# Performance work log

Hardware: AMD Instinct MI355X
Metric: run time of the kernel (lower is better)

## Reference

```python
import jax, jax.numpy as jnp
import numpy as np

FP8_MAX = 448.0  # float8_e4m3fn max
EPS = 1e-6


def _rms_norm(x, w):
    # x: [T, H], w: [H]
    var = jnp.mean(x * x, axis=-1, keepdims=True)
    return x * jax.lax.rsqrt(var + EPS) * w


def _fused_add_rms_norm(x, resid, w):
    r = x + resid
    return _rms_norm(r, w), r


def _fp8_linear(y, W):
    # dynamic per-token activation quant + per-tensor weight quant, fp8 e4m3
    s = jnp.maximum(jnp.max(jnp.abs(y), axis=-1, keepdims=True) / FP8_MAX, 1e-12)  # [T,1]
    qx = jnp.clip(y / s, -FP8_MAX, FP8_MAX).astype(jnp.float8_e4m3fn).astype(jnp.float32)
    ws = jnp.maximum(jnp.max(jnp.abs(W)) / FP8_MAX, 1e-12)  # scalar
    qw = jnp.clip(W / ws, -FP8_MAX, FP8_MAX).astype(jnp.float8_e4m3fn).astype(jnp.float32)
    # out = dequant(qx) @ dequant(qw).T = (qx @ qw.T) * s * ws ; W is [out, in]
    return (qx @ qw.T) * (s * ws)


def setup_inputs() -> dict:
    key = jax.random.key(0)
    ks = jax.random.split(key, 8)
    H, T = 4096, 4096
    x = jax.random.normal(ks[0], (T, H), dtype=jnp.float32)
    nw0 = 1.0 + 0.02 * jax.random.normal(ks[1], (H,), dtype=jnp.float32)
    nw1 = 1.0 + 0.02 * jax.random.normal(ks[2], (H,), dtype=jnp.float32)
    nw2 = 1.0 + 0.02 * jax.random.normal(ks[3], (H,), dtype=jnp.float32)
    nw3 = 1.0 + 0.02 * jax.random.normal(ks[4], (H,), dtype=jnp.float32)
    W0 = 0.02 * jax.random.normal(ks[5], (H, H), dtype=jnp.float32)
    W1 = 0.02 * jax.random.normal(ks[6], (H, H), dtype=jnp.float32)
    W2 = 0.02 * jax.random.normal(ks[7], (H, H), dtype=jnp.float32)
    return {"x": x, "nw0": nw0, "nw1": nw1, "nw2": nw2, "nw3": nw3,
            "W0": W0, "W1": W1, "W2": W2}


def reference(x, nw0, nw1, nw2, nw3, W0, W1, W2):
    x = jax.nn.relu(x)
    resid = x
    y = _rms_norm(x, nw0)
    x2 = _fp8_linear(y, W0)
    y2, resid = _fused_add_rms_norm(x2, resid, nw1)
    x3 = _fp8_linear(y2, W1)
    y3, resid = _fused_add_rms_norm(x3, resid, nw2)
    x4 = _fp8_linear(y3, W2)
    y4, resid = _fused_add_rms_norm(x4, resid, nw3)
    return y4
```

## Files before the change

### kernel.cpp

```cpp
#include <hip/hip_runtime.h>
#include <cstdint>
#include <cstddef>

#define AS1 __attribute__((address_space(1)))
#define AS3 __attribute__((address_space(3)))

typedef __attribute__((ext_vector_type(4))) float f32x4;
typedef __attribute__((ext_vector_type(16))) float f32x16;
typedef __attribute__((ext_vector_type(4))) int i32x4;
typedef __attribute__((ext_vector_type(8))) int i32x8;

constexpr int HD = 4096;
constexpr float FP8MAX = 448.0f;

__device__ inline float wave_red(float v, bool ismax) {
#pragma unroll
    for (int i = 32; i > 0; i >>= 1) {
        float o = __shfl_xor(v, i, 64);
        v = ismax ? fmaxf(v, o) : (v + o);
    }
    return v;
}

__device__ inline float blk_red(float v, float* red, bool ismax) {
    v = wave_red(v, ismax);
    const int wid = threadIdx.x >> 6;
    __syncthreads();
    if ((threadIdx.x & 63) == 0) red[wid] = v;
    __syncthreads();
    float a = red[0], b = red[1], c = red[2], d = red[3];
    return ismax ? fmaxf(fmaxf(a, b), fmaxf(c, d)) : ((a + b) + (c + d));
}

__device__ inline uint32_t pack4_fp8(float a, float b, float c, float d) {
    int v = 0;
    v = __builtin_amdgcn_cvt_pk_fp8_f32(a, b, v, false);
    v = __builtin_amdgcn_cvt_pk_fp8_f32(c, d, v, true);
    return (uint32_t)v;
}

__device__ inline float clipdiv(float y, float s) {
    float t = y / s;
    t = fminf(t, FP8MAX);
    t = fmaxf(t, -FP8MAX);
    return t;
}

__global__ __launch_bounds__(256) void w_absmax(const float* __restrict__ W0,
                                                const float* __restrict__ W1,
                                                const float* __restrict__ W2,
                                                uint32_t* __restrict__ wmax) {
    __shared__ float red[4];
    const float* W = (blockIdx.z == 0) ? W0 : (blockIdx.z == 1 ? W1 : W2);
    const float4* W4 = (const float4*)W;
    const int n4 = HD * HD / 4;
    float m = 0.f;
    for (int i = blockIdx.x * blockDim.x + threadIdx.x; i < n4; i += gridDim.x * blockDim.x) {
        float4 v = W4[i];
        m = fmaxf(m, fmaxf(fmaxf(fabsf(v.x), fabsf(v.y)), fmaxf(fabsf(v.z), fabsf(v.w))));
    }
    m = blk_red(m, red, true);
    if (threadIdx.x == 0)
        atomicMax((unsigned int*)(wmax + blockIdx.z), __float_as_uint(m));
}

__global__ __launch_bounds__(256) void w_quant(const float* __restrict__ W,
                                               const uint32_t* __restrict__ wmaxbits,
                                               uint32_t* __restrict__ qw) {
    const float sw = fmaxf(__uint_as_float(*wmaxbits) / FP8MAX, 1e-12f);
    const int i = blockIdx.x * blockDim.x + threadIdx.x;
    float4 v = ((const float4*)W)[i];
    qw[i] = pack4_fp8(clipdiv(v.x, sw), clipdiv(v.y, sw), clipdiv(v.z, sw), clipdiv(v.w, sw));
}

__global__ __launch_bounds__(256) void fused_rms(const float* __restrict__ xin,
                                                 const float* __restrict__ addin,
                                                 float* __restrict__ resid_out,
                                                 const float* __restrict__ nw,
                                                 uint32_t* __restrict__ qx,
                                                 float* __restrict__ srow,
                                                 float* __restrict__ yout,
                                                 const int mode) {
    __shared__ float red[4];
    const int row = blockIdx.x;
    const int tid = threadIdx.x;
    const size_t base = (size_t)row * HD;
    const float4* xr = (const float4*)(xin + base);

    float4 v[4];
    float ss = 0.f;
    if (mode == 0) {
#pragma unroll
        for (int j = 0; j < 4; j++) {
            float4 t = xr[tid + j * 256];
            t.x = fmaxf(t.x, 0.f); t.y = fmaxf(t.y, 0.f);
            t.z = fmaxf(t.z, 0.f); t.w = fmaxf(t.w, 0.f);
            v[j] = t;
            ss += t.x * t.x + t.y * t.y + t.z * t.z + t.w * t.w;
        }
    } else {
        const float4* ar = (const float4*)(addin + base);
#pragma unroll
        for (int j = 0; j < 4; j++) {
            float4 t = xr[tid + j * 256];
            float4 a = ar[tid + j * 256];
            t.x += a.x; t.y += a.y; t.z += a.z; t.w += a.w;
            v[j] = t;
            ss += t.x * t.x + t.y * t.y + t.z * t.z + t.w * t.w;
        }
    }
    if (resid_out) {
        float4* ro = (float4*)(resid_out + base);
#pragma unroll
        for (int j = 0; j < 4; j++) ro[tid + j * 256] = v[j];
    }
    ss = blk_red(ss, red, false);
    const float rs = 1.0f / sqrtf(ss / (float)HD + 1e-6f);

    const float4* nw4 = (const float4*)nw;
    float4 y[4];
    float amax = 0.f;
#pragma unroll
    for (int j = 0; j < 4; j++) {
        float4 w = nw4[tid + j * 256];
        float4 t;
        t.x = (v[j].x * rs) * w.x; t.y = (v[j].y * rs) * w.y;
        t.z = (v[j].z * rs) * w.z; t.w = (v[j].w * rs) * w.w;
        y[j] = t;
        amax = fmaxf(amax, fmaxf(fmaxf(fabsf(t.x), fabsf(t.y)), fmaxf(fabsf(t.z), fabsf(t.w))));
    }

    if (mode == 2) {
        float4* yo = (float4*)(yout + base);
#pragma unroll
        for (int j = 0; j < 4; j++) yo[tid + j * 256] = y[j];
        return;
    }

    amax = blk_red(amax, red, true);
    const float s = fmaxf(amax / FP8MAX, 1e-12f);
    if (tid == 0) srow[row] = s;
    uint32_t* qr = qx + base / 4;
#pragma unroll
    for (int j = 0; j < 4; j++) {
        qr[tid + j * 256] = pack4_fp8(clipdiv(y[j].x, s), clipdiv(y[j].y, s),
                                      clipdiv(y[j].z, s), clipdiv(y[j].w, s));
    }
}

__global__ __launch_bounds__(256) void gemm_fp8mx(const uint8_t* __restrict__ qx,
                                                  const uint8_t* __restrict__ qw,
                                                  const float* __restrict__ srow,
                                                  const uint32_t* __restrict__ wmaxbits,
                                                  float* __restrict__ out) {
    __shared__ uint8_t As[128 * 128];
    __shared__ uint8_t Bs[128 * 128];

    const int tid = threadIdx.x;
    const int wave = tid >> 6;
    const int lane = tid & 63;
    const int lr = lane & 31;
    const int lh = lane >> 5;

    const int m0 = blockIdx.y * 128;
    const int n0 = blockIdx.x * 128;
    const int wm = (wave >> 1) * 64;
    const int wn = (wave & 1) * 64;

    f32x16 acc[2][2];
#pragma unroll
    for (int i = 0; i < 2; i++)
#pragma unroll
        for (int j = 0; j < 2; j++)
#pragma unroll
            for (int e = 0; e < 16; e++) acc[i][j][e] = 0.f;

    const int strow = wave * 8 + (lane >> 3);
    const int sg = (lane & 7) ^ (lane >> 3);
    const uint8_t* aga = qx + (size_t)(m0 + strow) * HD + sg * 16;
    const uint8_t* bga = qw + (size_t)(n0 + strow) * HD + sg * 16;
    const int ldst = wave * 1024 + lane * 16;

    for (int k0 = 0; k0 < HD; k0 += 128) {
#pragma unroll
        for (int c = 0; c < 4; c++) {
            __builtin_amdgcn_global_load_lds((const AS1 void*)(aga + (size_t)c * 32 * HD + k0),
                                             (AS3 void*)(As + c * 4096 + ldst), 16, 0, 0);
            __builtin_amdgcn_global_load_lds((const AS1 void*)(bga + (size_t)c * 32 * HD + k0),
                                             (AS3 void*)(Bs + c * 4096 + ldst), 16, 0, 0);
        }
        __syncthreads();

#pragma unroll
        for (int kh = 0; kh < 2; kh++) {
            union { i32x8 v8; i32x4 v4[2]; } af[2], bf[2];
            const int kg0 = kh * 4 + lh * 2;
#pragma unroll
            for (int i = 0; i < 2; i++) {
                const int ar = wm + i * 32 + lr;
                const uint8_t* pa = As + ar * 128;
                af[i].v4[0] = *(const i32x4*)(pa + ((kg0 ^ (ar & 7)) << 4));
                af[i].v4[1] = *(const i32x4*)(pa + (((kg0 + 1) ^ (ar & 7)) << 4));
                const int br = wn + i * 32 + lr;
                const uint8_t* pb = Bs + br * 128;
                bf[i].v4[0] = *(const i32x4*)(pb + ((kg0 ^ (br & 7)) << 4));
                bf[i].v4[1] = *(const i32x4*)(pb + (((kg0 + 1) ^ (br & 7)) << 4));
            }
#pragma unroll
            for (int i = 0; i < 2; i++)
#pragma unroll
                for (int j = 0; j < 2; j++)
                    acc[i][j] = __builtin_amdgcn_mfma_scale_f32_32x32x64_f8f6f4(
                        af[i].v8, bf[j].v8, acc[i][j],
                        0, 0,
                        0, 0x7F7F7F7Fu,
                        0, 0x7F7F7F7Fu);
        }
        __syncthreads();
    }

    const float wsc = fmaxf(__uint_as_float(*wmaxbits) / FP8MAX, 1e-12f);
#pragma unroll
    for (int i = 0; i < 2; i++) {
#pragma unroll
        for (int reg = 0; reg < 16; reg++) {
            const int row = (reg & 3) + 8 * (reg >> 2) + 4 * lh;
            const int m = m0 + wm + i * 32 + row;
            const float sv = srow[m] * wsc;
            float* orow = out + (size_t)m * HD + n0 + wn + lr;
#pragma unroll
            for (int j = 0; j < 2; j++)
                orow[j * 32] = acc[i][j][reg] * sv;
        }
    }
}

extern "C" void kernel_launch(void* const* d_in, const int* in_sizes, int n_in,
                              void* d_out, int out_size, void* d_ws, size_t ws_size,
                              hipStream_t stream) {
    const float* x   = (const float*)d_in[0];
    const float* nw0 = (const float*)d_in[1];
    const float* nw1 = (const float*)d_in[2];
    const float* nw2 = (const float*)d_in[3];
    const float* nw3 = (const float*)d_in[4];
    const float* W0  = (const float*)d_in[5];
    const float* W1  = (const float*)d_in[6];
    const float* W2  = (const float*)d_in[7];
    float* out = (float*)d_out;

    char* ws = (char*)d_ws;
    float*    resid = (float*)(ws);
    uint32_t* qx    = (uint32_t*)(ws + (size_t)67108864);
    uint32_t* qw    = (uint32_t*)(ws + (size_t)83886080);
    float*    srow  = (float*)(ws + (size_t)100663296);
    uint32_t* wmax  = (uint32_t*)(ws + (size_t)100679680);
    float*    x2    = out;

    hipMemsetAsync(wmax, 0, 12, stream);
    hipLaunchKernelGGL(w_absmax, dim3(1024, 1, 3), dim3(256), 0, stream, W0, W1, W2, wmax);

    hipLaunchKernelGGL(fused_rms, dim3(4096), dim3(256), 0, stream,
                       x, (const float*)nullptr, resid, nw0, qx, srow, (float*)nullptr, 0);

    const float* Ws[3]  = {W0, W1, W2};
    const float* nws[3] = {nw1, nw2, nw3};
    for (int l = 0; l < 3; l++) {
        hipLaunchKernelGGL(w_quant, dim3(HD * HD / 4 / 256), dim3(256), 0, stream,
                           Ws[l], wmax + l, qw);
        hipLaunchKernelGGL(gemm_fp8mx, dim3(32, 32), dim3(256), 0, stream,
                           (const uint8_t*)qx, (const uint8_t*)qw, srow, wmax + l, x2);
        if (l < 2) {
            hipLaunchKernelGGL(fused_rms, dim3(4096), dim3(256), 0, stream,
                               x2, (const float*)resid, resid, nws[l], qx, srow,
                               (float*)nullptr, 1);
        } else {
            hipLaunchKernelGGL(fused_rms, dim3(4096), dim3(256), 0, stream,
                               x2, (const float*)resid, (float*)nullptr, nws[l],
                               (uint32_t*)nullptr, (float*)nullptr, out, 2);
        }
    }
}
```

Before: 657.3 us.

## Fold weight quantization into neighbouring kernels and merge RMS reductions

Weight fp8 quantization no longer runs as a separate launch. It is appended as extra blocks to the first RMS kernel (for W0) and to each GEMM grid (for the next layer's weight), with two ping-pong weight buffers, so it overlaps with useful work. The RMS kernel also computes the activation absmax in the same reduction pass as the sum of squares, using max|x*w|*rs. This removes one block-wide sync, and quantization multiplies by a reciprocal instead of dividing. The trade-offs are that division becomes reciprocal-multiply, which can change fp8 rounding at the edges, and the overlap path needs a larger workspace. When that workspace is not available it falls back to the old schedule.

```diff
diff --git a/kernel.cpp b/kernel.cpp
--- a/kernel.cpp
+++ b/kernel.cpp
@@ -12,25 +12,6 @@
 
 constexpr int HD = 4096;
 constexpr float FP8MAX = 448.0f;
-
-__device__ inline float wave_red(float v, bool ismax) {
-#pragma unroll
-    for (int i = 32; i > 0; i >>= 1) {
-        float o = __shfl_xor(v, i, 64);
-        v = ismax ? fmaxf(v, o) : (v + o);
-    }
-    return v;
-}
-
-__device__ inline float blk_red(float v, float* red, bool ismax) {
-    v = wave_red(v, ismax);
-    const int wid = threadIdx.x >> 6;
-    __syncthreads();
-    if ((threadIdx.x & 63) == 0) red[wid] = v;
-    __syncthreads();
-    float a = red[0], b = red[1], c = red[2], d = red[3];
-    return ismax ? fmaxf(fmaxf(a, b), fmaxf(c, d)) : ((a + b) + (c + d));
-}
 
 __device__ inline uint32_t pack4_fp8(float a, float b, float c, float d) {
     int v = 0;
@@ -39,11 +20,16 @@
     return (uint32_t)v;
 }
 
-__device__ inline float clipdiv(float y, float s) {
-    float t = y / s;
+__device__ inline float clipmul(float y, float rcs) {
+    float t = y * rcs;
     t = fminf(t, FP8MAX);
     t = fmaxf(t, -FP8MAX);
     return t;
+}
+
+__device__ inline uint32_t quant4(float4 v, float rcs) {
+    return pack4_fp8(clipmul(v.x, rcs), clipmul(v.y, rcs),
+                     clipmul(v.z, rcs), clipmul(v.w, rcs));
 }
 
 __global__ __launch_bounds__(256) void w_absmax(const float* __restrict__ W0,
@@ -59,18 +45,22 @@
         float4 v = W4[i];
         m = fmaxf(m, fmaxf(fmaxf(fabsf(v.x), fabsf(v.y)), fmaxf(fabsf(v.z), fabsf(v.w))));
     }
-    m = blk_red(m, red, true);
-    if (threadIdx.x == 0)
+#pragma unroll
+    for (int i = 32; i > 0; i >>= 1) m = fmaxf(m, __shfl_xor(m, i, 64));
+    if ((threadIdx.x & 63) == 0) red[threadIdx.x >> 6] = m;
+    __syncthreads();
+    if (threadIdx.x == 0) {
+        m = fmaxf(fmaxf(red[0], red[1]), fmaxf(red[2], red[3]));
         atomicMax((unsigned int*)(wmax + blockIdx.z), __float_as_uint(m));
+    }
 }
 
 __global__ __launch_bounds__(256) void w_quant(const float* __restrict__ W,
                                                const uint32_t* __restrict__ wmaxbits,
                                                uint32_t* __restrict__ qw) {
-    const float sw = fmaxf(__uint_as_float(*wmaxbits) / FP8MAX, 1e-12f);
+    const float rsw = 1.0f / fmaxf(__uint_as_float(*wmaxbits) / FP8MAX, 1e-12f);
     const int i = blockIdx.x * blockDim.x + threadIdx.x;
-    float4 v = ((const float4*)W)[i];
-    qw[i] = pack4_fp8(clipdiv(v.x, sw), clipdiv(v.y, sw), clipdiv(v.z, sw), clipdiv(v.w, sw));
+    qw[i] = quant4(((const float4*)W)[i], rsw);
 }
 
 __global__ __launch_bounds__(256) void fused_rms(const float* __restrict__ xin,
@@ -80,23 +70,41 @@
                                                  uint32_t* __restrict__ qx,
                                                  float* __restrict__ srow,
                                                  float* __restrict__ yout,
-                                                 const int mode) {
-    __shared__ float red[4];
+                                                 const int mode,
+                                                 const float* __restrict__ Wq,
+                                                 const uint32_t* __restrict__ wqmaxbits,
+                                                 uint32_t* __restrict__ qwout) {
+    const int tid = threadIdx.x;
+    if (blockIdx.x >= 4096) {
+        const float rsw = 1.0f / fmaxf(__uint_as_float(*wqmaxbits) / FP8MAX, 1e-12f);
+        const float4* W4 = (const float4*)Wq;
+        int i = (blockIdx.x - 4096) * 256 + tid;
+#pragma unroll
+        for (int it = 0; it < 4; it++, i += 4096 * 256)
+            qwout[i] = quant4(W4[i], rsw);
+        return;
+    }
+
+    __shared__ float reds[4];
+    __shared__ float redm[4];
     const int row = blockIdx.x;
-    const int tid = threadIdx.x;
     const size_t base = (size_t)row * HD;
     const float4* xr = (const float4*)(xin + base);
-
-    float4 v[4];
-    float ss = 0.f;
+    const float4* nw4 = (const float4*)nw;
+
+    float4 v[4], w[4];
+    float ss = 0.f, pm = 0.f;
     if (mode == 0) {
 #pragma unroll
         for (int j = 0; j < 4; j++) {
             float4 t = xr[tid + j * 256];
+            w[j] = nw4[tid + j * 256];
             t.x = fmaxf(t.x, 0.f); t.y = fmaxf(t.y, 0.f);
             t.z = fmaxf(t.z, 0.f); t.w = fmaxf(t.w, 0.f);
             v[j] = t;
             ss += t.x * t.x + t.y * t.y + t.z * t.z + t.w * t.w;
+            pm = fmaxf(pm, fmaxf(fmaxf(fabsf(t.x * w[j].x), fabsf(t.y * w[j].y)),
+                                 fmaxf(fabsf(t.z * w[j].z), fabsf(t.w * w[j].w))));
         }
     } else {
         const float4* ar = (const float4*)(addin + base);
@@ -104,9 +112,12 @@
         for (int j = 0; j < 4; j++) {
             float4 t = xr[tid + j * 256];
             float4 a = ar[tid + j * 256];
+            w[j] = nw4[tid + j * 256];
             t.x += a.x; t.y += a.y; t.z += a.z; t.w += a.w;
             v[j] = t;
             ss += t.x * t.x + t.y * t.y + t.z * t.z + t.w * t.w;
+            pm = fmaxf(pm, fmaxf(fmaxf(fabsf(t.x * w[j].x), fabsf(t.y * w[j].y)),
+                                 fmaxf(fabsf(t.z * w[j].z), fabsf(t.w * w[j].w))));
         }
     }
     if (resid_out) {
@@ -114,37 +125,42 @@
 #pragma unroll
         for (int j = 0; j < 4; j++) ro[tid + j * 256] = v[j];
     }
-    ss = blk_red(ss, red, false);
+
+#pragma unroll
+    for (int i = 32; i > 0; i >>= 1) {
+        ss += __shfl_xor(ss, i, 64);
+        pm = fmaxf(pm, __shfl_xor(pm, i, 64));
+    }
+    if ((tid & 63) == 0) { reds[tid >> 6] = ss; redm[tid >> 6] = pm; }
+    __syncthreads();
+    ss = (reds[0] + reds[1]) + (reds[2] + reds[3]);
+    pm = fmaxf(fmaxf(redm[0], redm[1]), fmaxf(redm[2], redm[3]));
+
     const float rs = 1.0f / sqrtf(ss / (float)HD + 1e-6f);
-
-    const float4* nw4 = (const float4*)nw;
-    float4 y[4];
-    float amax = 0.f;
-#pragma unroll
-    for (int j = 0; j < 4; j++) {
-        float4 w = nw4[tid + j * 256];
-        float4 t;
-        t.x = (v[j].x * rs) * w.x; t.y = (v[j].y * rs) * w.y;
-        t.z = (v[j].z * rs) * w.z; t.w = (v[j].w * rs) * w.w;
-        y[j] = t;
-        amax = fmaxf(amax, fmaxf(fmaxf(fabsf(t.x), fabsf(t.y)), fmaxf(fabsf(t.z), fabsf(t.w))));
-    }
 
     if (mode == 2) {
         float4* yo = (float4*)(yout + base);
 #pragma unroll
-        for (int j = 0; j < 4; j++) yo[tid + j * 256] = y[j];
+        for (int j = 0; j < 4; j++) {
+            float4 t;
+            t.x = (v[j].x * rs) * w[j].x; t.y = (v[j].y * rs) * w[j].y;
+            t.z = (v[j].z * rs) * w[j].z; t.w = (v[j].w * rs) * w[j].w;
+            yo[tid + j * 256] = t;
+        }
         return;
     }
 
-    amax = blk_red(amax, red, true);
+    const float amax = pm * rs;
     const float s = fmaxf(amax / FP8MAX, 1e-12f);
+    const float rcs = 1.0f / s;
     if (tid == 0) srow[row] = s;
     uint32_t* qr = qx + base / 4;
 #pragma unroll
     for (int j = 0; j < 4; j++) {
-        qr[tid + j * 256] = pack4_fp8(clipdiv(y[j].x, s), clipdiv(y[j].y, s),
-                                      clipdiv(y[j].z, s), clipdiv(y[j].w, s));
+        float4 t;
+        t.x = (v[j].x * rs) * w[j].x; t.y = (v[j].y * rs) * w[j].y;
+        t.z = (v[j].z * rs) * w[j].z; t.w = (v[j].w * rs) * w[j].w;
+        qr[tid + j * 256] = quant4(t, rcs);
     }
 }
 
@@ -152,11 +168,25 @@
                                                   const uint8_t* __restrict__ qw,
                                                   const float* __restrict__ srow,
                                                   const uint32_t* __restrict__ wmaxbits,
-                                                  float* __restrict__ out) {
+                                                  float* __restrict__ out,
+                                                  const float* __restrict__ Wnext,
+                                                  const uint32_t* __restrict__ wnmaxbits,
+                                                  uint32_t* __restrict__ qwnext) {
     __shared__ uint8_t As[128 * 128];
     __shared__ uint8_t Bs[128 * 128];
 
     const int tid = threadIdx.x;
+
+    if (blockIdx.z == 1) {
+        const float rsw = 1.0f / fmaxf(__uint_as_float(*wnmaxbits) / FP8MAX, 1e-12f);
+        const float4* W4 = (const float4*)Wnext;
+        int i = (blockIdx.y * 32 + blockIdx.x) * 256 + tid;
+#pragma unroll
+        for (int it = 0; it < 16; it++, i += 1024 * 256)
+            qwnext[i] = quant4(W4[i], rsw);
+        return;
+    }
+
     const int wave = tid >> 6;
     const int lane = tid & 63;
     const int lr = lane & 31;
@@ -249,34 +279,75 @@
     float* out = (float*)d_out;
 
     char* ws = (char*)d_ws;
-    float*    resid = (float*)(ws);
-    uint32_t* qx    = (uint32_t*)(ws + (size_t)67108864);
-    uint32_t* qw    = (uint32_t*)(ws + (size_t)83886080);
-    float*    srow  = (float*)(ws + (size_t)100663296);
-    uint32_t* wmax  = (uint32_t*)(ws + (size_t)100679680);
-    float*    x2    = out;
-
-    hipMemsetAsync(wmax, 0, 12, stream);
-    hipLaunchKernelGGL(w_absmax, dim3(1024, 1, 3), dim3(256), 0, stream, W0, W1, W2, wmax);
-
-    hipLaunchKernelGGL(fused_rms, dim3(4096), dim3(256), 0, stream,
-                       x, (const float*)nullptr, resid, nw0, qx, srow, (float*)nullptr, 0);
-
-    const float* Ws[3]  = {W0, W1, W2};
-    const float* nws[3] = {nw1, nw2, nw3};
-    for (int l = 0; l < 3; l++) {
-        hipLaunchKernelGGL(w_quant, dim3(HD * HD / 4 / 256), dim3(256), 0, stream,
-                           Ws[l], wmax + l, qw);
-        hipLaunchKernelGGL(gemm_fp8mx, dim3(32, 32), dim3(256), 0, stream,
-                           (const uint8_t*)qx, (const uint8_t*)qw, srow, wmax + l, x2);
-        if (l < 2) {
-            hipLaunchKernelGGL(fused_rms, dim3(4096), dim3(256), 0, stream,
-                               x2, (const float*)resid, resid, nws[l], qx, srow,
-                               (float*)nullptr, 1);
-        } else {
-            hipLaunchKernelGGL(fused_rms, dim3(4096), dim3(256), 0, stream,
-                               x2, (const float*)resid, (float*)nullptr, nws[l],
-                               (uint32_t*)nullptr, (float*)nullptr, out, 2);
-        }
-    }
-}
+    const size_t MB = 1024 * 1024;
+    float* x2 = out;
+
+    const bool overlap = ws_size >= 118 * MB;
+
+    if (overlap) {
+        float*    resid = (float*)(ws);
+        uint32_t* qx    = (uint32_t*)(ws + 64 * MB);
+        uint32_t* qwA   = (uint32_t*)(ws + 80 * MB);
+        uint32_t* qwB   = (uint32_t*)(ws + 96 * MB);
+        float*    srow  = (float*)(ws + 112 * MB);
+        uint32_t* wmax  = (uint32_t*)(ws + 112 * MB + 16384);
+
+        hipMemsetAsync(wmax, 0, 12, stream);
+        hipLaunchKernelGGL(w_absmax, dim3(1024, 1, 3), dim3(256), 0, stream, W0, W1, W2, wmax);
+
+        hipLaunchKernelGGL(fused_rms, dim3(8192), dim3(256), 0, stream,
+                           x, (const float*)nullptr, resid, nw0, qx, srow, (float*)nullptr, 0,
+                           W0, wmax + 0, qwA);
+        hipLaunchKernelGGL(gemm_fp8mx, dim3(32, 32, 2), dim3(256), 0, stream,
+                           (const uint8_t*)qx, (const uint8_t*)qwA, srow, wmax + 0, x2,
+                           W1, wmax + 1, qwB);
+        hipLaunchKernelGGL(fused_rms, dim3(4096), dim3(256), 0, stream,
+                           x2, (const float*)resid, resid, nw1, qx, srow, (float*)nullptr, 1,
+                           (const float*)nullptr, (const uint32_t*)nullptr, (uint32_t*)nullptr);
+        hipLaunchKernelGGL(gemm_fp8mx, dim3(32, 32, 2), dim3(256), 0, stream,
+                           (const uint8_t*)qx, (const uint8_t*)qwB, srow, wmax + 1, x2,
+                           W2, wmax + 2, qwA);
+        hipLaunchKernelGGL(fused_rms, dim3(4096), dim3(256), 0, stream,
+                           x2, (const float*)resid, resid, nw2, qx, srow, (float*)nullptr, 1,
+                           (const float*)nullptr, (const uint32_t*)nullptr, (uint32_t*)nullptr);
+        hipLaunchKernelGGL(gemm_fp8mx, dim3(32, 32, 1), dim3(256), 0, stream,
+                           (const uint8_t*)qx, (const uint8_t*)qwA, srow, wmax + 2, x2,
+                           (const float*)nullptr, (const uint32_t*)nullptr, (uint32_t*)nullptr);
+        hipLaunchKernelGGL(fused_rms, dim3(4096), dim3(256), 0, stream,
+                           x2, (const float*)resid, (float*)nullptr, nw3,
+                           (uint32_t*)nullptr, (float*)nullptr, out, 2,
+                           (const float*)nullptr, (const uint32_t*)nullptr, (uint32_t*)nullptr);
+    } else {
+        float*    resid = (float*)(ws);
+        uint32_t* qx    = (uint32_t*)(ws + 64 * MB);
+        uint32_t* qw    = (uint32_t*)(ws + 80 * MB);
+        float*    srow  = (float*)(ws + 96 * MB);
+        uint32_t* wmax  = (uint32_t*)(ws + 96 * MB + 16384);
+
+        hipMemsetAsync(wmax, 0, 12, stream);
+        hipLaunchKernelGGL(w_absmax, dim3(1024, 1, 3), dim3(256), 0, stream, W0, W1, W2, wmax);
+        hipLaunchKernelGGL(fused_rms, dim3(4096), dim3(256), 0, stream,
+                           x, (const float*)nullptr, resid, nw0, qx, srow, (float*)nullptr, 0,
+                           (const float*)nullptr, (const uint32_t*)nullptr, (uint32_t*)nullptr);
+        const float* Ws[3]  = {W0, W1, W2};
+        const float* nws[3] = {nw1, nw2, nw3};
+        for (int l = 0; l < 3; l++) {
+            hipLaunchKernelGGL(w_quant, dim3(HD * HD / 4 / 256), dim3(256), 0, stream,
+                               Ws[l], wmax + l, qw);
+            hipLaunchKernelGGL(gemm_fp8mx, dim3(32, 32, 1), dim3(256), 0, stream,
+                               (const uint8_t*)qx, (const uint8_t*)qw, srow, wmax + l, x2,
+                               (const float*)nullptr, (const uint32_t*)nullptr, (uint32_t*)nullptr);
+            if (l < 2) {
+                hipLaunchKernelGGL(fused_rms, dim3(4096), dim3(256), 0, stream,
+                                   x2, (const float*)resid, resid, nws[l], qx, srow,
+                                   (float*)nullptr, 1,
+                                   (const float*)nullptr, (const uint32_t*)nullptr, (uint32_t*)nullptr);
+            } else {
+                hipLaunchKernelGGL(fused_rms, dim3(4096), dim3(256), 0, stream,
+                                   x2, (const float*)resid, (float*)nullptr, nws[l],
+                                   (uint32_t*)nullptr, (float*)nullptr, out, 2,
+                                   (const float*)nullptr, (const uint32_t*)nullptr, (uint32_t*)nullptr);
+            }
+        }
+    }
+}
```

Measured after the change: 647.8 us. No clear change (-1.5%).
